# Performance work log

Hardware: AMD Instinct MI355X
Metric: run time of the kernel (lower is better)

Reference implementation:

```python
import jax, jax.numpy as jnp
import numpy as np

B, T = 64, 64
HUMAN, IN = 64, 8
HS, ES, K = 1024, 1024, 7
PSI_H, PSI_LR = 1024, 30

_PAR_SHAPES = [(HS, HS), (HS,), (IN, HS), (HS, HUMAN), (IN, HUMAN - IN)]
_PAR_SIZES = [int(np.prod(s)) for s in _PAR_SHAPES]
N_PSI = int(sum(_PAR_SIZES))
_OFFS = np.cumsum([0] + _PAR_SIZES)


def setup_inputs() -> dict:
    key = jax.random.key(0)
    ks = jax.random.split(key, 16)
    def xav(k, shape):
        lim = float(np.sqrt(6.0 / (shape[0] + shape[1])))
        return jax.random.uniform(k, shape, minval=-lim, maxval=lim, dtype=jnp.float32)
    def uni(k, shape, s):
        return jax.random.uniform(k, shape, minval=-s, maxval=s, dtype=jnp.float32)
    se = float(1.0 / np.sqrt(ES))
    return {
        "inputs": jax.random.normal(ks[0], (B, T, IN), jnp.float32),
        "outputs": jax.random.normal(ks[1], (B, T, HUMAN), jnp.float32),
        "eps": jax.random.normal(ks[2], (B, K), jnp.float32),
        "enc_Wih": uni(ks[3], (3 * ES, HUMAN), se),
        "enc_Whh": uni(ks[4], (3 * ES, ES), se),
        "enc_bih": uni(ks[5], (3 * ES,), se),
        "enc_bhh": uni(ks[6], (3 * ES,), se),
        "to_mu": xav(ks[7], (ES, K)),
        "to_lsigma": xav(ks[8], (ES, K)),
        "to_lsigma_bias": -0.5 * jnp.ones((K,), jnp.float32),
        "W1": xav(ks[9], (K, PSI_H)),
        "b1": jnp.zeros((PSI_H,), jnp.float32),
        "W2": xav(ks[10], (PSI_H, PSI_LR)),
        "b2": jnp.zeros((PSI_LR,), jnp.float32),
        "W3": xav(ks[11], (PSI_LR, N_PSI)),
        "b3": jnp.zeros((N_PSI,), jnp.float32),
        "gru_Wih": xav(ks[12], (IN, 2 * HS)),
        "gru_Whh": xav(ks[13], (HS, 2 * HS)),
        "gru_bias": jnp.concatenate([jnp.zeros((HS,)), jnp.ones((HS,))]).astype(jnp.float32),
    }


def _gru_cell(h, x, Wih, Whh, bih, bhh):
    # torch.nn.GRUCell math, gate order (r, z, n)
    gx = x @ Wih.T + bih
    gh = h @ Whh.T + bhh
    xr, xz, xn = jnp.split(gx, 3, axis=-1)
    hr, hz, hn = jnp.split(gh, 3, axis=-1)
    r = jax.nn.sigmoid(xr + hr)
    z = jax.nn.sigmoid(xz + hz)
    n = jnp.tanh(xn + r * hn)
    return (1.0 - z) * n + z * h


def _split_psi(psi):
    # psi: [B, N_PSI] -> per-sample (Whh, bh, Wih, C, D)
    return [psi[:, _OFFS[i]:_OFFS[i + 1]].reshape((-1,) + _PAR_SHAPES[i]) for i in range(5)]


def reference(inputs, outputs, eps, enc_Wih, enc_Whh, enc_bih, enc_bhh,
              to_mu, to_lsigma, to_lsigma_bias, W1, b1, W2, b2, W3, b3,
              gru_Wih, gru_Whh, gru_bias):
    bsz = inputs.shape[0]
    # ---- encoder: GRUCell over time-major outputs ----
    out_tm = jnp.swapaxes(outputs, 0, 1)  # [T, B, HUMAN]
    h0 = jnp.zeros((bsz, ES), inputs.dtype)
    h_enc = _gru_cell(h0, out_tm[0], enc_Wih, enc_Whh, enc_bih, enc_bhh)
    def enc_step(h, x):
        h = _gru_cell(h, x, enc_Wih, enc_Whh, enc_bih, enc_bhh)
        return h, None
    h_enc, _ = jax.lax.scan(enc_step, h_enc, out_tm[1:])
    mu = h_enc @ to_mu                       # [B, K]
    logstd = h_enc @ to_lsigma + to_lsigma_bias
    z = mu + eps * jnp.exp(logstd)
    # ---- hypernetwork psi decoder ----
    psi = (jnp.tanh(z @ W1 + b1) @ W2 + b2) @ W3 + b3   # [B, N_PSI]
    Whh_b, bh_b, Wih_b, C_b, D_b = _split_psi(psi)
    # ---- per-sample GRU decoder, vectorized over batch, scan over time ----
    gx_all = jnp.einsum('bti,ij->tbj', inputs, gru_Wih)  # [T, B, 2*HS]
    xW_all = jnp.einsum('bti,bih->tbh', inputs, Wih_b)   # [T, B, HS]

    def dec_step(h, xs):
        gx_t, xW_t = xs
        pre = gx_t + h @ gru_Whh + gru_bias   # [B, 2*HS]
        z_t = jax.nn.sigmoid(pre[:, :HS])
        r_t = jax.nn.sigmoid(pre[:, HS:])
        hWhh = jnp.einsum('bh,bhk->bk', h, Whh_b) + bh_b
        eta = jnp.tanh(xW_t + r_t * jnp.tanh(hWhh))
        h_new = z_t * h + (1.0 - z_t) * eta
        return h_new, h_new

    state0 = jnp.zeros((bsz, HS), inputs.dtype)
    h_last, dec_seq = jax.lax.scan(dec_step, state0, (gx_all, xW_all))
    dec_seq = jnp.swapaxes(dec_seq, 0, 1)    # [B, T, HS]
    # ---- readout ----
    yhats = jnp.einsum('bth,bhm->btm', dec_seq, C_b)
    xD = jnp.einsum('bti,bim->btm', inputs, D_b)  # [B, T, HUMAN-IN]
    yhats = yhats + jnp.concatenate([jnp.zeros_like(inputs), xD], axis=-1)
    # residual output
    yhats = yhats + jnp.concatenate(
        [inputs, jnp.zeros((bsz, inputs.shape[1], HUMAN - IN), inputs.dtype)], axis=-1)
    states = jax.lax.stop_gradient(h_last)
    return yhats, mu, logstd, states
```

## Files before the change

### kernel.cpp

```cpp
#include <hip/hip_runtime.h>

namespace {
constexpr int nT = 64;
constexpr int nK = 7;
constexpr long N_PSI = 1123776;
constexpr long SZ_WHH = 1048576;
constexpr long REST_SZ = 75200;
constexpr long R_BH = 0;
constexpr long R_WIH = 1024;
constexpr long R_C = 9216;
constexpr long R_D = 74752;
constexpr int NCH = 32;
constexpr int CHR = 32;
constexpr long PHALF = (long)NCH * 64 * 1024;
}

typedef __attribute__((ext_vector_type(4))) unsigned short us4;
typedef __attribute__((ext_vector_type(2))) unsigned short us2;

__device__ __forceinline__ float b2f(unsigned short u) {
  return __uint_as_float(((unsigned int)u) << 16);
}
__device__ __forceinline__ unsigned short f2b(float f) {
  unsigned int u = __float_as_uint(f);
  return (unsigned short)((u + 0x7fffu + ((u >> 16) & 1u)) >> 16);
}
__device__ __forceinline__ float sigm(float x) { return 1.f / (1.f + __expf(-x)); }

__global__ void transpose_bf16_k(const float* __restrict__ in, unsigned short* __restrict__ out,
                                 int rows, int cols) {
  __shared__ float tile[32][33];
  int x = blockIdx.x * 32 + threadIdx.x;
  int y = blockIdx.y * 32 + threadIdx.y;
  #pragma unroll
  for (int i = 0; i < 32; i += 8)
    if ((y + i) < rows && x < cols) tile[threadIdx.y + i][threadIdx.x] = in[(long)(y + i) * cols + x];
  __syncthreads();
  x = blockIdx.y * 32 + threadIdx.x;
  y = blockIdx.x * 32 + threadIdx.y;
  #pragma unroll
  for (int i = 0; i < 32; i += 8)
    if ((y + i) < cols && x < rows) out[(long)(y + i) * rows + x] = f2b(tile[threadIdx.x][threadIdx.y + i]);
}

__global__ void cvt_bf16_k(const float* __restrict__ in, unsigned short* __restrict__ out, long n) {
  long i = (long)blockIdx.x * 256 + threadIdx.x;
  if (i < n) out[i] = f2b(in[i]);
}

__global__ __launch_bounds__(256) void enc_gx_k(const float* __restrict__ outputs,
                                                const unsigned short* __restrict__ WtWihB,
                                                const float* __restrict__ bih,
                                                unsigned short* __restrict__ gxE) {
  int g0 = blockIdx.x * 256;
  int btg = blockIdx.y;
  __shared__ unsigned short ws[64 * 256];
  __shared__ float xs[64][64];
  for (int i = threadIdx.x; i < 64 * 256; i += 256)
    ws[i] = WtWihB[(long)(i >> 8) * 3072 + g0 + (i & 255)];
  for (int i = threadIdx.x; i < 64 * 64; i += 256) {
    int idx = btg * 64 + (i >> 6);
    int t = idx >> 6, b = idx & 63;
    xs[i >> 6][i & 63] = outputs[((long)b * nT + t) * 64 + (i & 63)];
  }
  __syncthreads();
  float bihv = bih[g0 + threadIdx.x];
  for (int j = 0; j < 64; ++j) {
    int idx = btg * 64 + j;
    float acc = bihv;
    #pragma unroll 8
    for (int i = 0; i < 64; ++i) acc += xs[j][i] * b2f(ws[i * 256 + threadIdx.x]);
    gxE[(long)idx * 3072 + g0 + threadIdx.x] = f2b(acc);
  }
}

__global__ __launch_bounds__(256) void dec_gx_k(const float* __restrict__ inputs,
                                                const float* __restrict__ gWih,
                                                const float* __restrict__ gbias,
                                                unsigned short* __restrict__ gxD) {
  int g0 = blockIdx.x * 256;
  int btg = blockIdx.y;
  __shared__ float ws[8][256];
  __shared__ float xs[64][8];
  for (int i = threadIdx.x; i < 8 * 256; i += 256)
    ws[i >> 8][i & 255] = gWih[(long)(i >> 8) * 2048 + g0 + (i & 255)];
  for (int i = threadIdx.x; i < 64 * 8; i += 256) {
    int idx = btg * 64 + (i >> 3);
    int t = idx >> 6, b = idx & 63;
    xs[i >> 3][i & 7] = inputs[((long)b * nT + t) * 8 + (i & 7)];
  }
  __syncthreads();
  float bv = gbias[g0 + threadIdx.x];
  for (int j = 0; j < 64; ++j) {
    int idx = btg * 64 + j;
    float acc = bv;
    #pragma unroll
    for (int i = 0; i < 8; ++i) acc += xs[j][i] * ws[i][threadIdx.x];
    gxD[(long)idx * 2048 + g0 + threadIdx.x] = f2b(acc);
  }
}

__global__ __launch_bounds__(256) void xW_k(const float* __restrict__ inputs,
                                            const float* __restrict__ Rest,
                                            unsigned short* __restrict__ xWb) {
  int k0 = blockIdx.x * 256;
  int b = blockIdx.y;
  __shared__ float ws[8][256];
  __shared__ float xs[64][8];
  const float* RB = Rest + (long)b * REST_SZ + R_WIH;
  for (int i = threadIdx.x; i < 8 * 256; i += 256)
    ws[i >> 8][i & 255] = RB[(long)(i >> 8) * 1024 + k0 + (i & 255)];
  for (int i = threadIdx.x; i < 64 * 8; i += 256)
    xs[i >> 3][i & 7] = inputs[((long)b * nT + (i >> 3)) * 8 + (i & 7)];
  __syncthreads();
  for (int t = 0; t < 64; ++t) {
    float acc = 0.f;
    #pragma unroll
    for (int i = 0; i < 8; ++i) acc += xs[t][i] * ws[i][threadIdx.x];
    xWb[((long)t * 64 + b) * 1024 + k0 + threadIdx.x] = f2b(acc);
  }
}

__global__ __launch_bounds__(256) void enc_step_k(
    const unsigned short* __restrict__ W,
    const unsigned short* __restrict__ gxE,
    const float* __restrict__ bhh,
    float* __restrict__ hEnc,
    const float* __restrict__ pRr, const float* __restrict__ pZr, const float* __restrict__ pNr,
    float* __restrict__ pRw, float* __restrict__ pZw, float* __restrict__ pNw,
    int t) {
  int c = blockIdx.x & (NCH - 1);
  int sp = blockIdx.x >> 5;
  int b0 = sp * 2, b1 = b0 + 1;
  __shared__ float h0s[CHR], h1s[CHR];
  __shared__ float redR[4][64], redZ[4][64], redN[4][64];

  int v = threadIdx.x;
  int q = v >> 6, idx = v & 63;
  {
    int hi = idx >> 5, e_in = idx & 31;
    int bb = hi ? b1 : b0;
    int e = c * CHR + e_in;
    float sr = 0.f, sz = 0.f, sn = 0.f;
    if (t > 0) {
      #pragma unroll
      for (int cc = q * 8; cc < q * 8 + 8; ++cc) {
        long base = ((long)cc * 64 + bb) * 1024 + e;
        sr += pRr[base]; sz += pZr[base]; sn += pNr[base];
      }
    }
    redR[q][idx] = sr; redZ[q][idx] = sz; redN[q][idx] = sn;
  }
  __syncthreads();
  if (v < 64) {
    int hi = v >> 5, e_in = v & 31;
    int bb = hi ? b1 : b0;
    int e = c * CHR + e_in;
    float sr = redR[0][v] + redR[1][v] + redR[2][v] + redR[3][v];
    float sz = redZ[0][v] + redZ[1][v] + redZ[2][v] + redZ[3][v];
    float sn = redN[0][v] + redN[1][v] + redN[2][v] + redN[3][v];
    long gb = ((long)t * 64 + bb) * 3072;
    float xr = b2f(gxE[gb + e]), xz = b2f(gxE[gb + 1024 + e]), xn = b2f(gxE[gb + 2048 + e]);
    float hr = sr + bhh[e], hz = sz + bhh[1024 + e], hn = sn + bhh[2048 + e];
    float r = sigm(xr + hr);
    float z = sigm(xz + hz);
    float n = tanhf(xn + r * hn);
    float hold = (t > 0) ? hEnc[(long)bb * 1024 + e] : 0.f;
    float hnew = (1.f - z) * n + z * hold;
    hEnc[(long)bb * 1024 + e] = hnew;
    if (hi) h1s[e_in] = hnew; else h0s[e_in] = hnew;
  }
  __syncthreads();

  if (t < nT - 1) {
    int e0 = threadIdx.x * 4;
    float ar0[4] = {}, az0[4] = {}, an0[4] = {}, ar1[4] = {}, az1[4] = {}, an1[4] = {};
    const unsigned short* Wb = W + (long)(c * CHR) * 3072 + e0;
    #pragma unroll 4
    for (int j = 0; j < CHR; ++j) {
      us4 wr = *(const us4*)(Wb + (long)j * 3072);
      us4 wz = *(const us4*)(Wb + (long)j * 3072 + 1024);
      us4 wn = *(const us4*)(Wb + (long)j * 3072 + 2048);
      float hv0 = h0s[j], hv1 = h1s[j];
      #pragma unroll
      for (int qq = 0; qq < 4; ++qq) {
        float fr = b2f(wr[qq]), fz = b2f(wz[qq]), fn = b2f(wn[qq]);
        ar0[qq] += hv0 * fr; az0[qq] += hv0 * fz; an0[qq] += hv0 * fn;
        ar1[qq] += hv1 * fr; az1[qq] += hv1 * fz; an1[qq] += hv1 * fn;
      }
    }
    long i0 = ((long)c * 64 + b0) * 1024 + e0;
    long i1 = i0 + 1024;
    *(float4*)(pRw + i0) = make_float4(ar0[0], ar0[1], ar0[2], ar0[3]);
    *(float4*)(pZw + i0) = make_float4(az0[0], az0[1], az0[2], az0[3]);
    *(float4*)(pNw + i0) = make_float4(an0[0], an0[1], an0[2], an0[3]);
    *(float4*)(pRw + i1) = make_float4(ar1[0], ar1[1], ar1[2], ar1[3]);
    *(float4*)(pZw + i1) = make_float4(az1[0], az1[1], az1[2], az1[3]);
    *(float4*)(pNw + i1) = make_float4(an1[0], an1[1], an1[2], an1[3]);
  }
}

__global__ __launch_bounds__(256) void latent_hyper_k(
    const float* __restrict__ h_enc,
    const float* __restrict__ to_mu, const float* __restrict__ to_lsig,
    const float* __restrict__ lsig_bias, const float* __restrict__ eps,
    const float* __restrict__ W1, const float* __restrict__ b1,
    const float* __restrict__ W2, const float* __restrict__ b2,
    float* __restrict__ out_mu, float* __restrict__ out_lsig,
    float* __restrict__ a2out) {
  int b = blockIdx.x;
  __shared__ float hs[1024];
  __shared__ float zv[8];
  __shared__ float a1[1024];
  for (int i = threadIdx.x; i < 1024; i += 256) hs[i] = h_enc[b * 1024 + i];
  __syncthreads();
  int g = threadIdx.x >> 5, s = threadIdx.x & 31;
  if (g < nK) {
    float am = 0.f, as_ = 0.f;
    for (int h = s; h < 1024; h += 32) {
      float hv = hs[h];
      am += hv * to_mu[h * nK + g];
      as_ += hv * to_lsig[h * nK + g];
    }
    #pragma unroll
    for (int m = 16; m >= 1; m >>= 1) { am += __shfl_xor(am, m); as_ += __shfl_xor(as_, m); }
    if (s == 0) {
      float ls = as_ + lsig_bias[g];
      out_mu[b * nK + g] = am;
      out_lsig[b * nK + g] = ls;
      zv[g] = am + eps[b * nK + g] * __expf(ls);
    }
  }
  __syncthreads();
  for (int j = threadIdx.x; j < 1024; j += 256) {
    float acc = b1[j];
    #pragma unroll
    for (int i = 0; i < nK; ++i) acc += zv[i] * W1[i * 1024 + j];
    a1[j] = tanhf(acc);
  }
  __syncthreads();
  int l = threadIdx.x >> 3, s8 = threadIdx.x & 7;
  if (l < 30) {
    float acc = 0.f;
    for (int j = s8; j < 1024; j += 8) acc += a1[j] * W2[j * 30 + l];
    acc += __shfl_xor(acc, 4);
    acc += __shfl_xor(acc, 2);
    acc += __shfl_xor(acc, 1);
    if (s8 == 0) a2out[b * 30 + l] = acc + b2[l];
  }
}

__global__ __launch_bounds__(256) void psi_k(const float* __restrict__ a2,
                                             const float* __restrict__ W3, const float* __restrict__ b3,
                                             unsigned short* __restrict__ WhhB, float* __restrict__ Rest) {
  __shared__ float sa[64 * 30];
  for (int i = threadIdx.x; i < 64 * 30; i += 256) sa[i] = a2[i];
  long n0 = ((long)blockIdx.x * 256 + threadIdx.x) * 2;
  __syncthreads();
  if (n0 >= N_PSI) return;
  float2 w[30];
  #pragma unroll
  for (int l = 0; l < 30; ++l) w[l] = *(const float2*)(W3 + (long)l * N_PSI + n0);
  float2 bb = *(const float2*)(b3 + n0);
  bool isWhh = (n0 < SZ_WHH);
  for (int b = 0; b < 64; ++b) {
    float a0 = bb.x, a1v = bb.y;
    const float* ab = &sa[b * 30];
    #pragma unroll
    for (int l = 0; l < 30; ++l) { float av = ab[l]; a0 += av * w[l].x; a1v += av * w[l].y; }
    if (isWhh) {
      us2 o; o[0] = f2b(a0); o[1] = f2b(a1v);
      *(us2*)(WhhB + (long)b * SZ_WHH + n0) = o;
    } else {
      *(float2*)(Rest + (long)b * REST_SZ + (n0 - SZ_WHH)) = make_float2(a0, a1v);
    }
  }
}

__global__ __launch_bounds__(256) void dec_step_k(
    const unsigned short* __restrict__ WhhB,
    const unsigned short* __restrict__ gWhhB,
    const unsigned short* __restrict__ gxD,
    const unsigned short* __restrict__ xWb,
    const float* __restrict__ Rest,
    float* __restrict__ decS,
    const float* __restrict__ pZr, const float* __restrict__ pRr, const float* __restrict__ pWr,
    float* __restrict__ pZw, float* __restrict__ pRw, float* __restrict__ pWw,
    int t) {
  int c = blockIdx.x & (NCH - 1);
  int sp = blockIdx.x >> 5;
  int b0 = sp * 2, b1 = b0 + 1;
  __shared__ float h0s[CHR], h1s[CHR];
  __shared__ float redZ[4][64], redR[4][64], redW[4][64];

  int v = threadIdx.x;
  int q = v >> 6, idx = v & 63;
  {
    int hi = idx >> 5, e_in = idx & 31;
    int bb = hi ? b1 : b0;
    int k = c * CHR + e_in;
    float sz = 0.f, sr = 0.f, sw = 0.f;
    if (t > 0) {
      #pragma unroll
      for (int cc = q * 8; cc < q * 8 + 8; ++cc) {
        long base = ((long)cc * 64 + bb) * 1024 + k;
        sz += pZr[base]; sr += pRr[base]; sw += pWr[base];
      }
    }
    redZ[q][idx] = sz; redR[q][idx] = sr; redW[q][idx] = sw;
  }
  __syncthreads();
  if (v < 64) {
    int hi = v >> 5, e_in = v & 31;
    int bb = hi ? b1 : b0;
    int k = c * CHR + e_in;
    float sz = redZ[0][v] + redZ[1][v] + redZ[2][v] + redZ[3][v];
    float sr = redR[0][v] + redR[1][v] + redR[2][v] + redR[3][v];
    float sw = redW[0][v] + redW[1][v] + redW[2][v] + redW[3][v];
    long gb = ((long)t * 64 + bb) * 2048;
    float gz = b2f(gxD[gb + k]), gr = b2f(gxD[gb + 1024 + k]);
    float z = sigm(gz + sz);
    float r = sigm(gr + sr);
    float hW = sw + Rest[(long)bb * REST_SZ + R_BH + k];
    float xw = b2f(xWb[((long)t * 64 + bb) * 1024 + k]);
    float eta = tanhf(xw + r * tanhf(hW));
    float hold = (t > 0) ? decS[((long)bb * nT + (t - 1)) * 1024 + k] : 0.f;
    float hnew = z * hold + (1.f - z) * eta;
    decS[((long)bb * nT + t) * 1024 + k] = hnew;
    if (hi) h1s[e_in] = hnew; else h0s[e_in] = hnew;
  }
  __syncthreads();

  if (t < nT - 1) {
    int k0 = threadIdx.x * 4;
    float az0[4] = {}, ar0[4] = {}, aw0[4] = {}, az1[4] = {}, ar1[4] = {}, aw1[4] = {};
    const unsigned short* G = gWhhB + (long)(c * CHR) * 2048 + k0;
    const unsigned short* W0 = WhhB + (long)b0 * SZ_WHH + (long)(c * CHR) * 1024 + k0;
    const unsigned short* W1p = WhhB + (long)b1 * SZ_WHH + (long)(c * CHR) * 1024 + k0;
    #pragma unroll 4
    for (int j = 0; j < CHR; ++j) {
      us4 wz = *(const us4*)(G + (long)j * 2048);
      us4 wr = *(const us4*)(G + (long)j * 2048 + 1024);
      us4 w0 = *(const us4*)(W0 + (long)j * 1024);
      us4 w1 = *(const us4*)(W1p + (long)j * 1024);
      float hv0 = h0s[j], hv1 = h1s[j];
      #pragma unroll
      for (int qq = 0; qq < 4; ++qq) {
        float fz = b2f(wz[qq]), fr = b2f(wr[qq]), f0 = b2f(w0[qq]), f1 = b2f(w1[qq]);
        az0[qq] += hv0 * fz; ar0[qq] += hv0 * fr; aw0[qq] += hv0 * f0;
        az1[qq] += hv1 * fz; ar1[qq] += hv1 * fr; aw1[qq] += hv1 * f1;
      }
    }
    long i0 = ((long)c * 64 + b0) * 1024 + k0;
    long i1 = i0 + 1024;
    *(float4*)(pZw + i0) = make_float4(az0[0], az0[1], az0[2], az0[3]);
    *(float4*)(pRw + i0) = make_float4(ar0[0], ar0[1], ar0[2], ar0[3]);
    *(float4*)(pWw + i0) = make_float4(aw0[0], aw0[1], aw0[2], aw0[3]);
    *(float4*)(pZw + i1) = make_float4(az1[0], az1[1], az1[2], az1[3]);
    *(float4*)(pRw + i1) = make_float4(ar1[0], ar1[1], ar1[2], ar1[3]);
    *(float4*)(pWw + i1) = make_float4(aw1[0], aw1[1], aw1[2], aw1[3]);
  }
}

__global__ __launch_bounds__(256) void readout_k(
    const float* __restrict__ dec_seq, const float* __restrict__ inputs,
    const float* __restrict__ Rest, float* __restrict__ yhats) {
  int b = blockIdx.x >> 3;
  int tg = blockIdx.x & 7;
  __shared__ float ss[8][1024];
  __shared__ float part[4][8][64];
  for (int i = threadIdx.x; i < 8 * 1024; i += 256)
    ss[i >> 10][i & 1023] = dec_seq[((long)b * nT + tg * 8 + (i >> 10)) * 1024 + (i & 1023)];
  __syncthreads();
  int m = threadIdx.x & 63, hq = threadIdx.x >> 6;
  const float* C = Rest + (long)b * REST_SZ + R_C;
  float acc[8] = {};
  for (int h = hq * 256; h < hq * 256 + 256; ++h) {
    float cv = C[(long)h * 64 + m];
    #pragma unroll
    for (int tt = 0; tt < 8; ++tt) acc[tt] += ss[tt][h] * cv;
  }
  #pragma unroll
  for (int tt = 0; tt < 8; ++tt) part[hq][tt][m] = acc[tt];
  __syncthreads();
  const float* D = Rest + (long)b * REST_SZ + R_D;
  for (int o = threadIdx.x; o < 512; o += 256) {
    int tt = o >> 6, mm = o & 63;
    float a = part[0][tt][mm] + part[1][tt][mm] + part[2][tt][mm] + part[3][tt][mm];
    long bt = (long)b * nT + tg * 8 + tt;
    if (mm < 8) {
      a += inputs[bt * 8 + mm];
    } else {
      #pragma unroll
      for (int i = 0; i < 8; ++i) a += inputs[bt * 8 + i] * D[i * 56 + (mm - 8)];
    }
    yhats[bt * 64 + mm] = a;
  }
}

__global__ void copy_states_k(const float* __restrict__ dec_seq, float* __restrict__ states) {
  int i = blockIdx.x * 256 + threadIdx.x;
  int b = i >> 10, h = i & 1023;
  states[i] = dec_seq[((long)b * nT + (nT - 1)) * 1024 + h];
}

extern "C" void kernel_launch(void* const* d_in, const int* in_sizes, int n_in,
                              void* d_out, int out_size, void* d_ws, size_t ws_size,
                              hipStream_t stream) {
  const float* inputs  = (const float*)d_in[0];
  const float* outputs = (const float*)d_in[1];
  const float* eps     = (const float*)d_in[2];
  const float* enc_Wih = (const float*)d_in[3];
  const float* enc_Whh = (const float*)d_in[4];
  const float* enc_bih = (const float*)d_in[5];
  const float* enc_bhh = (const float*)d_in[6];
  const float* to_mu   = (const float*)d_in[7];
  const float* to_lsig = (const float*)d_in[8];
  const float* lsig_b  = (const float*)d_in[9];
  const float* W1 = (const float*)d_in[10];
  const float* b1 = (const float*)d_in[11];
  const float* W2 = (const float*)d_in[12];
  const float* b2 = (const float*)d_in[13];
  const float* W3 = (const float*)d_in[14];
  const float* b3 = (const float*)d_in[15];
  const float* gWih  = (const float*)d_in[16];
  const float* gWhh  = (const float*)d_in[17];
  const float* gbias = (const float*)d_in[18];

  char* ws = (char*)d_ws;
  size_t off = 0;
  auto alloc = [&](size_t bytes) { size_t o = off; off = (off + bytes + 255) & ~(size_t)255; return o; };
  size_t oWhhB   = alloc(64ull * SZ_WHH * 2);
  size_t oRest   = alloc(64ull * REST_SZ * 4);
  size_t ogWhhB  = alloc(1024ull * 2048 * 2);
  size_t oWtWhhB = alloc(1024ull * 3072 * 2);
  size_t oWtWihB = alloc(64ull * 3072 * 2);
  size_t ogxE    = alloc(64ull * 64 * 3072 * 2);
  size_t ogxD    = alloc(64ull * 64 * 2048 * 2);
  size_t oxWb    = alloc(64ull * 64 * 1024 * 2);
  size_t opA     = alloc((size_t)2 * PHALF * 4);
  size_t opB     = alloc((size_t)2 * PHALF * 4);
  size_t opC     = alloc((size_t)2 * PHALF * 4);
  size_t ohA     = alloc(64ull * 1024 * 4);
  size_t oDec    = alloc(64ull * 64 * 1024 * 4);
  size_t oZ      = alloc(64 * nK * 4);
  size_t oA2     = alloc(64 * 30 * 4);
  (void)ws_size; (void)in_sizes; (void)n_in; (void)out_size; (void)oZ;

  unsigned short* WhhB   = (unsigned short*)(ws + oWhhB);
  float*          Rest   = (float*)(ws + oRest);
  unsigned short* gWhhB  = (unsigned short*)(ws + ogWhhB);
  unsigned short* WtWhhB = (unsigned short*)(ws + oWtWhhB);
  unsigned short* WtWihB = (unsigned short*)(ws + oWtWihB);
  unsigned short* gxE    = (unsigned short*)(ws + ogxE);
  unsigned short* gxD    = (unsigned short*)(ws + ogxD);
  unsigned short* xWb    = (unsigned short*)(ws + oxWb);
  float* pA   = (float*)(ws + opA);
  float* pB   = (float*)(ws + opB);
  float* pC   = (float*)(ws + opC);
  float* hA   = (float*)(ws + ohA);
  float* decS = (float*)(ws + oDec);
  float* a2   = (float*)(ws + oA2);

  float* out    = (float*)d_out;
  float* out_yh = out;
  float* out_mu = out + 262144;
  float* out_ls = out + 262144 + 448;
  float* out_st = out + 262144 + 896;

  transpose_bf16_k<<<dim3(32, 96), dim3(32, 8), 0, stream>>>(enc_Whh, WtWhhB, 3072, 1024);
  transpose_bf16_k<<<dim3(2, 96),  dim3(32, 8), 0, stream>>>(enc_Wih, WtWihB, 3072, 64);
  cvt_bf16_k<<<(int)((1024ull * 2048 + 255) / 256), 256, 0, stream>>>(gWhh, gWhhB, 1024 * 2048);

  enc_gx_k<<<dim3(12, 64), 256, 0, stream>>>(outputs, WtWihB, enc_bih, gxE);

  for (int t = 0; t < nT; ++t) {
    int rp = t & 1, wp = (t + 1) & 1;
    enc_step_k<<<1024, 256, 0, stream>>>(WtWhhB, gxE, enc_bhh, hA,
        pA + (size_t)rp * PHALF, pB + (size_t)rp * PHALF, pC + (size_t)rp * PHALF,
        pA + (size_t)wp * PHALF, pB + (size_t)wp * PHALF, pC + (size_t)wp * PHALF, t);
  }

  latent_hyper_k<<<64, 256, 0, stream>>>(hA, to_mu, to_lsig, lsig_b, eps,
                                         W1, b1, W2, b2, out_mu, out_ls, a2);
  psi_k<<<(int)((N_PSI / 2 + 255) / 256), 256, 0, stream>>>(a2, W3, b3, WhhB, Rest);

  dec_gx_k<<<dim3(8, 64), 256, 0, stream>>>(inputs, gWih, gbias, gxD);
  xW_k<<<dim3(4, 64), 256, 0, stream>>>(inputs, Rest, xWb);

  for (int t = 0; t < nT; ++t) {
    int rp = t & 1, wp = (t + 1) & 1;
    dec_step_k<<<1024, 256, 0, stream>>>(WhhB, gWhhB, gxD, xWb, Rest, decS,
        pA + (size_t)rp * PHALF, pB + (size_t)rp * PHALF, pC + (size_t)rp * PHALF,
        pA + (size_t)wp * PHALF, pB + (size_t)wp * PHALF, pC + (size_t)wp * PHALF, t);
  }

  readout_k<<<512, 256, 0, stream>>>(decS, inputs, Rest, out_yh);
  copy_states_k<<<256, 256, 0, stream>>>(decS, out_st);
}
```

Measured before the change: 3.401 ms.

## Quantize per-sample decoder Whh to int8 and retile recurrent step kernels

The generated per-sample recurrent weight matrix Whh goes from bf16 to int8, with one scale per (sample, input row). The scales come from a separate max-abs pass over the hypernetwork output, and the scale is folded into h before the matvec. This halves the bytes streamed for the dominant per-step weight read in the decoder. Both encoder and decoder step kernels also move from 32 chunks of 32 rows at 256 threads to 16 chunks of 64 rows at 512 threads, with gate work split across two thread halves, which halves the partial-sum traffic. The cost is an extra psi pass that recomputes the hypernetwork matmul, plus quantization error in the decoder weights.

```diff
diff --git a/kernel.cpp b/kernel.cpp
--- a/kernel.cpp
+++ b/kernel.cpp
@@ -10,13 +10,11 @@
 constexpr long R_WIH = 1024;
 constexpr long R_C = 9216;
 constexpr long R_D = 74752;
-constexpr int NCH = 32;
-constexpr int CHR = 32;
+constexpr int NCH = 16;
 constexpr long PHALF = (long)NCH * 64 * 1024;
 }
 
 typedef __attribute__((ext_vector_type(4))) unsigned short us4;
-typedef __attribute__((ext_vector_type(2))) unsigned short us2;
 
 __device__ __forceinline__ float b2f(unsigned short u) {
   return __uint_as_float(((unsigned int)u) << 16);
@@ -121,7 +119,7 @@
   }
 }
 
-__global__ __launch_bounds__(256) void enc_step_k(
+__global__ __launch_bounds__(512, 2) void enc_step3_k(
     const unsigned short* __restrict__ W,
     const unsigned short* __restrict__ gxE,
     const float* __restrict__ bhh,
@@ -130,35 +128,33 @@
     float* __restrict__ pRw, float* __restrict__ pZw, float* __restrict__ pNw,
     int t) {
   int c = blockIdx.x & (NCH - 1);
-  int sp = blockIdx.x >> 5;
+  int sp = blockIdx.x >> 4;
   int b0 = sp * 2, b1 = b0 + 1;
-  __shared__ float h0s[CHR], h1s[CHR];
-  __shared__ float redR[4][64], redZ[4][64], redN[4][64];
-
+  __shared__ float h0s[64], h1s[64];
+  __shared__ float red[3][4][128];
   int v = threadIdx.x;
-  int q = v >> 6, idx = v & 63;
   {
-    int hi = idx >> 5, e_in = idx & 31;
-    int bb = hi ? b1 : b0;
-    int e = c * CHR + e_in;
+    int q = v >> 7, idx = v & 127;
+    int bb = (idx >> 6) ? b1 : b0;
+    int e = c * 64 + (idx & 63);
     float sr = 0.f, sz = 0.f, sn = 0.f;
     if (t > 0) {
       #pragma unroll
-      for (int cc = q * 8; cc < q * 8 + 8; ++cc) {
+      for (int cc = q * 4; cc < q * 4 + 4; ++cc) {
         long base = ((long)cc * 64 + bb) * 1024 + e;
         sr += pRr[base]; sz += pZr[base]; sn += pNr[base];
       }
     }
-    redR[q][idx] = sr; redZ[q][idx] = sz; redN[q][idx] = sn;
-  }
-  __syncthreads();
-  if (v < 64) {
-    int hi = v >> 5, e_in = v & 31;
+    red[0][q][idx] = sr; red[1][q][idx] = sz; red[2][q][idx] = sn;
+  }
+  __syncthreads();
+  if (v < 128) {
+    int hi = v >> 6;
     int bb = hi ? b1 : b0;
-    int e = c * CHR + e_in;
-    float sr = redR[0][v] + redR[1][v] + redR[2][v] + redR[3][v];
-    float sz = redZ[0][v] + redZ[1][v] + redZ[2][v] + redZ[3][v];
-    float sn = redN[0][v] + redN[1][v] + redN[2][v] + redN[3][v];
+    int e = c * 64 + (v & 63);
+    float sr = red[0][0][v] + red[0][1][v] + red[0][2][v] + red[0][3][v];
+    float sz = red[1][0][v] + red[1][1][v] + red[1][2][v] + red[1][3][v];
+    float sn = red[2][0][v] + red[2][1][v] + red[2][2][v] + red[2][3][v];
     long gb = ((long)t * 64 + bb) * 3072;
     float xr = b2f(gxE[gb + e]), xz = b2f(gxE[gb + 1024 + e]), xn = b2f(gxE[gb + 2048 + e]);
     float hr = sr + bhh[e], hz = sz + bhh[1024 + e], hn = sn + bhh[2048 + e];
@@ -168,35 +164,51 @@
     float hold = (t > 0) ? hEnc[(long)bb * 1024 + e] : 0.f;
     float hnew = (1.f - z) * n + z * hold;
     hEnc[(long)bb * 1024 + e] = hnew;
-    if (hi) h1s[e_in] = hnew; else h0s[e_in] = hnew;
-  }
-  __syncthreads();
-
+    if (hi) h1s[v & 63] = hnew; else h0s[v & 63] = hnew;
+  }
+  __syncthreads();
   if (t < nT - 1) {
-    int e0 = threadIdx.x * 4;
-    float ar0[4] = {}, az0[4] = {}, an0[4] = {}, ar1[4] = {}, az1[4] = {}, an1[4] = {};
-    const unsigned short* Wb = W + (long)(c * CHR) * 3072 + e0;
-    #pragma unroll 4
-    for (int j = 0; j < CHR; ++j) {
-      us4 wr = *(const us4*)(Wb + (long)j * 3072);
-      us4 wz = *(const us4*)(Wb + (long)j * 3072 + 1024);
-      us4 wn = *(const us4*)(Wb + (long)j * 3072 + 2048);
-      float hv0 = h0s[j], hv1 = h1s[j];
-      #pragma unroll
-      for (int qq = 0; qq < 4; ++qq) {
-        float fr = b2f(wr[qq]), fz = b2f(wz[qq]), fn = b2f(wn[qq]);
-        ar0[qq] += hv0 * fr; az0[qq] += hv0 * fz; an0[qq] += hv0 * fn;
-        ar1[qq] += hv1 * fr; az1[qq] += hv1 * fz; an1[qq] += hv1 * fn;
+    if (v < 256) {
+      int e0 = v * 4;
+      float ar0[4] = {}, az0[4] = {}, ar1[4] = {}, az1[4] = {};
+      const unsigned short* Wb = W + (long)(c * 64) * 3072 + e0;
+      #pragma unroll 4
+      for (int j = 0; j < 64; ++j) {
+        us4 wr = *(const us4*)(Wb + (long)j * 3072);
+        us4 wz = *(const us4*)(Wb + (long)j * 3072 + 1024);
+        float hv0 = h0s[j], hv1 = h1s[j];
+        #pragma unroll
+        for (int q = 0; q < 4; ++q) {
+          float fr = b2f(wr[q]), fz = b2f(wz[q]);
+          ar0[q] += hv0 * fr; az0[q] += hv0 * fz;
+          ar1[q] += hv1 * fr; az1[q] += hv1 * fz;
+        }
       }
-    }
-    long i0 = ((long)c * 64 + b0) * 1024 + e0;
-    long i1 = i0 + 1024;
-    *(float4*)(pRw + i0) = make_float4(ar0[0], ar0[1], ar0[2], ar0[3]);
-    *(float4*)(pZw + i0) = make_float4(az0[0], az0[1], az0[2], az0[3]);
-    *(float4*)(pNw + i0) = make_float4(an0[0], an0[1], an0[2], an0[3]);
-    *(float4*)(pRw + i1) = make_float4(ar1[0], ar1[1], ar1[2], ar1[3]);
-    *(float4*)(pZw + i1) = make_float4(az1[0], az1[1], az1[2], az1[3]);
-    *(float4*)(pNw + i1) = make_float4(an1[0], an1[1], an1[2], an1[3]);
+      long i0 = ((long)c * 64 + b0) * 1024 + e0;
+      long i1 = i0 + 1024;
+      *(float4*)(pRw + i0) = make_float4(ar0[0], ar0[1], ar0[2], ar0[3]);
+      *(float4*)(pZw + i0) = make_float4(az0[0], az0[1], az0[2], az0[3]);
+      *(float4*)(pRw + i1) = make_float4(ar1[0], ar1[1], ar1[2], ar1[3]);
+      *(float4*)(pZw + i1) = make_float4(az1[0], az1[1], az1[2], az1[3]);
+    } else {
+      int e0 = (v - 256) * 4;
+      float an0[4] = {}, an1[4] = {};
+      const unsigned short* Wb = W + (long)(c * 64) * 3072 + 2048 + e0;
+      #pragma unroll 8
+      for (int j = 0; j < 64; ++j) {
+        us4 wn = *(const us4*)(Wb + (long)j * 3072);
+        float hv0 = h0s[j], hv1 = h1s[j];
+        #pragma unroll
+        for (int q = 0; q < 4; ++q) {
+          float fn = b2f(wn[q]);
+          an0[q] += hv0 * fn; an1[q] += hv1 * fn;
+        }
+      }
+      long i0 = ((long)c * 64 + b0) * 1024 + e0;
+      long i1 = i0 + 1024;
+      *(float4*)(pNw + i0) = make_float4(an0[0], an0[1], an0[2], an0[3]);
+      *(float4*)(pNw + i1) = make_float4(an1[0], an1[1], an1[2], an1[3]);
+    }
   }
 }
 
@@ -250,35 +262,84 @@
   }
 }
 
-__global__ __launch_bounds__(256) void psi_k(const float* __restrict__ a2,
-                                             const float* __restrict__ W3, const float* __restrict__ b3,
-                                             unsigned short* __restrict__ WhhB, float* __restrict__ Rest) {
+__global__ __launch_bounds__(256) void psi_max_k(
+    const float* __restrict__ a2, const float* __restrict__ W3, const float* __restrict__ b3,
+    unsigned* __restrict__ pmax) {
+  __shared__ float sa[64 * 30];
+  __shared__ float wm[4][64];
+  for (int i = threadIdx.x; i < 64 * 30; i += 256) sa[i] = a2[i];
+  long n0 = (long)blockIdx.x * 256 + threadIdx.x;
+  int h = (int)(n0 >> 10);
+  __syncthreads();
+  float acc[64];
+  float bb = b3[n0];
+  #pragma unroll
+  for (int b = 0; b < 64; ++b) acc[b] = bb;
+  for (int l = 0; l < 30; ++l) {
+    float w = W3[(long)l * N_PSI + n0];
+    #pragma unroll
+    for (int b = 0; b < 64; ++b) acc[b] += sa[b * 30 + l] * w;
+  }
+  int lane = threadIdx.x & 63, wv = threadIdx.x >> 6;
+  #pragma unroll
+  for (int b = 0; b < 64; ++b) {
+    float m = fabsf(acc[b]);
+    #pragma unroll
+    for (int d = 32; d >= 1; d >>= 1) m = fmaxf(m, __shfl_xor(m, d));
+    if (lane == 0) wm[wv][b] = m;
+  }
+  __syncthreads();
+  if (threadIdx.x < 64) {
+    int b = threadIdx.x;
+    float m = fmaxf(fmaxf(wm[0][b], wm[1][b]), fmaxf(wm[2][b], wm[3][b]));
+    atomicMax(&pmax[b * 1024 + h], __float_as_uint(m));
+  }
+}
+
+__global__ void wscale2_k(const unsigned* __restrict__ pmax,
+                          float* __restrict__ sdec, float* __restrict__ sinv) {
+  int i = blockIdx.x * 256 + threadIdx.x;
+  float m = __uint_as_float(pmax[i]);
+  sdec[i] = m / 127.f;
+  sinv[i] = (m > 0.f) ? 127.f / m : 0.f;
+}
+
+__global__ __launch_bounds__(256) void psi_q_k(
+    const float* __restrict__ a2, const float* __restrict__ W3, const float* __restrict__ b3,
+    const float* __restrict__ sinv, char* __restrict__ Q8, float* __restrict__ Rest) {
   __shared__ float sa[64 * 30];
   for (int i = threadIdx.x; i < 64 * 30; i += 256) sa[i] = a2[i];
-  long n0 = ((long)blockIdx.x * 256 + threadIdx.x) * 2;
+  long n0 = (long)blockIdx.x * 256 + threadIdx.x;
   __syncthreads();
   if (n0 >= N_PSI) return;
-  float2 w[30];
+  float acc[64];
+  float bb = b3[n0];
   #pragma unroll
-  for (int l = 0; l < 30; ++l) w[l] = *(const float2*)(W3 + (long)l * N_PSI + n0);
-  float2 bb = *(const float2*)(b3 + n0);
-  bool isWhh = (n0 < SZ_WHH);
-  for (int b = 0; b < 64; ++b) {
-    float a0 = bb.x, a1v = bb.y;
-    const float* ab = &sa[b * 30];
-    #pragma unroll
-    for (int l = 0; l < 30; ++l) { float av = ab[l]; a0 += av * w[l].x; a1v += av * w[l].y; }
-    if (isWhh) {
-      us2 o; o[0] = f2b(a0); o[1] = f2b(a1v);
-      *(us2*)(WhhB + (long)b * SZ_WHH + n0) = o;
-    } else {
-      *(float2*)(Rest + (long)b * REST_SZ + (n0 - SZ_WHH)) = make_float2(a0, a1v);
-    }
-  }
-}
-
-__global__ __launch_bounds__(256) void dec_step_k(
-    const unsigned short* __restrict__ WhhB,
+  for (int b = 0; b < 64; ++b) acc[b] = bb;
+  for (int l = 0; l < 30; ++l) {
+    float w = W3[(long)l * N_PSI + n0];
+    #pragma unroll
+    for (int b = 0; b < 64; ++b) acc[b] += sa[b * 30 + l] * w;
+  }
+  if (n0 < SZ_WHH) {
+    int h = (int)(n0 >> 10);
+    const float* si = sinv + h;
+    #pragma unroll
+    for (int b = 0; b < 64; ++b) {
+      int q = __float2int_rn(acc[b] * si[b * 1024]);
+      q = min(127, max(-127, q));
+      Q8[(long)b * SZ_WHH + n0] = (char)q;
+    }
+  } else {
+    long r = n0 - SZ_WHH;
+    #pragma unroll
+    for (int b = 0; b < 64; ++b) Rest[(long)b * REST_SZ + r] = acc[b];
+  }
+}
+
+__global__ __launch_bounds__(512, 2) void dec_step_q8d_k(
+    const char* __restrict__ Q8,
+    const float* __restrict__ sdec,
     const unsigned short* __restrict__ gWhhB,
     const unsigned short* __restrict__ gxD,
     const unsigned short* __restrict__ xWb,
@@ -288,35 +349,34 @@
     float* __restrict__ pZw, float* __restrict__ pRw, float* __restrict__ pWw,
     int t) {
   int c = blockIdx.x & (NCH - 1);
-  int sp = blockIdx.x >> 5;
+  int sp = blockIdx.x >> 4;
   int b0 = sp * 2, b1 = b0 + 1;
-  __shared__ float h0s[CHR], h1s[CHR];
-  __shared__ float redZ[4][64], redR[4][64], redW[4][64];
-
+  __shared__ float h0s[64], h1s[64];
+  __shared__ float h0q[64], h1q[64];
+  __shared__ float red[3][4][128];
   int v = threadIdx.x;
-  int q = v >> 6, idx = v & 63;
   {
-    int hi = idx >> 5, e_in = idx & 31;
-    int bb = hi ? b1 : b0;
-    int k = c * CHR + e_in;
+    int q = v >> 7, idx = v & 127;
+    int bb = (idx >> 6) ? b1 : b0;
+    int k = c * 64 + (idx & 63);
     float sz = 0.f, sr = 0.f, sw = 0.f;
     if (t > 0) {
       #pragma unroll
-      for (int cc = q * 8; cc < q * 8 + 8; ++cc) {
+      for (int cc = q * 4; cc < q * 4 + 4; ++cc) {
         long base = ((long)cc * 64 + bb) * 1024 + k;
         sz += pZr[base]; sr += pRr[base]; sw += pWr[base];
       }
     }
-    redZ[q][idx] = sz; redR[q][idx] = sr; redW[q][idx] = sw;
-  }
-  __syncthreads();
-  if (v < 64) {
-    int hi = v >> 5, e_in = v & 31;
+    red[0][q][idx] = sz; red[1][q][idx] = sr; red[2][q][idx] = sw;
+  }
+  __syncthreads();
+  if (v < 128) {
+    int hi = v >> 6;
     int bb = hi ? b1 : b0;
-    int k = c * CHR + e_in;
-    float sz = redZ[0][v] + redZ[1][v] + redZ[2][v] + redZ[3][v];
-    float sr = redR[0][v] + redR[1][v] + redR[2][v] + redR[3][v];
-    float sw = redW[0][v] + redW[1][v] + redW[2][v] + redW[3][v];
+    int k = c * 64 + (v & 63);
+    float sz = red[0][0][v] + red[0][1][v] + red[0][2][v] + red[0][3][v];
+    float sr = red[1][0][v] + red[1][1][v] + red[1][2][v] + red[1][3][v];
+    float sw = red[2][0][v] + red[2][1][v] + red[2][2][v] + red[2][3][v];
     long gb = ((long)t * 64 + bb) * 2048;
     float gz = b2f(gxD[gb + k]), gr = b2f(gxD[gb + 1024 + k]);
     float z = sigm(gz + sz);
@@ -327,38 +387,54 @@
     float hold = (t > 0) ? decS[((long)bb * nT + (t - 1)) * 1024 + k] : 0.f;
     float hnew = z * hold + (1.f - z) * eta;
     decS[((long)bb * nT + t) * 1024 + k] = hnew;
-    if (hi) h1s[e_in] = hnew; else h0s[e_in] = hnew;
-  }
-  __syncthreads();
-
+    float hsc = hnew * sdec[(long)bb * 1024 + k];
+    if (hi) { h1s[v & 63] = hnew; h1q[v & 63] = hsc; }
+    else    { h0s[v & 63] = hnew; h0q[v & 63] = hsc; }
+  }
+  __syncthreads();
   if (t < nT - 1) {
-    int k0 = threadIdx.x * 4;
-    float az0[4] = {}, ar0[4] = {}, aw0[4] = {}, az1[4] = {}, ar1[4] = {}, aw1[4] = {};
-    const unsigned short* G = gWhhB + (long)(c * CHR) * 2048 + k0;
-    const unsigned short* W0 = WhhB + (long)b0 * SZ_WHH + (long)(c * CHR) * 1024 + k0;
-    const unsigned short* W1p = WhhB + (long)b1 * SZ_WHH + (long)(c * CHR) * 1024 + k0;
-    #pragma unroll 4
-    for (int j = 0; j < CHR; ++j) {
-      us4 wz = *(const us4*)(G + (long)j * 2048);
-      us4 wr = *(const us4*)(G + (long)j * 2048 + 1024);
-      us4 w0 = *(const us4*)(W0 + (long)j * 1024);
-      us4 w1 = *(const us4*)(W1p + (long)j * 1024);
-      float hv0 = h0s[j], hv1 = h1s[j];
-      #pragma unroll
-      for (int qq = 0; qq < 4; ++qq) {
-        float fz = b2f(wz[qq]), fr = b2f(wr[qq]), f0 = b2f(w0[qq]), f1 = b2f(w1[qq]);
-        az0[qq] += hv0 * fz; ar0[qq] += hv0 * fr; aw0[qq] += hv0 * f0;
-        az1[qq] += hv1 * fz; ar1[qq] += hv1 * fr; aw1[qq] += hv1 * f1;
+    if (v < 256) {
+      int k0 = v * 4;
+      float az0[4] = {}, ar0[4] = {}, az1[4] = {}, ar1[4] = {};
+      const unsigned short* G = gWhhB + (long)(c * 64) * 2048 + k0;
+      #pragma unroll 4
+      for (int j = 0; j < 64; ++j) {
+        us4 wz = *(const us4*)(G + (long)j * 2048);
+        us4 wr = *(const us4*)(G + (long)j * 2048 + 1024);
+        float hv0 = h0s[j], hv1 = h1s[j];
+        #pragma unroll
+        for (int q = 0; q < 4; ++q) {
+          float fz = b2f(wz[q]), fr = b2f(wr[q]);
+          az0[q] += hv0 * fz; ar0[q] += hv0 * fr;
+          az1[q] += hv1 * fz; ar1[q] += hv1 * fr;
+        }
       }
-    }
-    long i0 = ((long)c * 64 + b0) * 1024 + k0;
-    long i1 = i0 + 1024;
-    *(float4*)(pZw + i0) = make_float4(az0[0], az0[1], az0[2], az0[3]);
-    *(float4*)(pRw + i0) = make_float4(ar0[0], ar0[1], ar0[2], ar0[3]);
-    *(float4*)(pWw + i0) = make_float4(aw0[0], aw0[1], aw0[2], aw0[3]);
-    *(float4*)(pZw + i1) = make_float4(az1[0], az1[1], az1[2], az1[3]);
-    *(float4*)(pRw + i1) = make_float4(ar1[0], ar1[1], ar1[2], ar1[3]);
-    *(float4*)(pWw + i1) = make_float4(aw1[0], aw1[1], aw1[2], aw1[3]);
+      long i0 = ((long)c * 64 + b0) * 1024 + k0;
+      long i1 = i0 + 1024;
+      *(float4*)(pZw + i0) = make_float4(az0[0], az0[1], az0[2], az0[3]);
+      *(float4*)(pRw + i0) = make_float4(ar0[0], ar0[1], ar0[2], ar0[3]);
+      *(float4*)(pZw + i1) = make_float4(az1[0], az1[1], az1[2], az1[3]);
+      *(float4*)(pRw + i1) = make_float4(ar1[0], ar1[1], ar1[2], ar1[3]);
+    } else {
+      int k0 = (v - 256) * 4;
+      float aw0[4] = {}, aw1[4] = {};
+      const char* Q0 = Q8 + (long)b0 * SZ_WHH + (long)(c * 64) * 1024 + k0;
+      const char* Q1 = Q8 + (long)b1 * SZ_WHH + (long)(c * 64) * 1024 + k0;
+      #pragma unroll 8
+      for (int j = 0; j < 64; ++j) {
+        char4 q0 = *(const char4*)(Q0 + (long)j * 1024);
+        char4 q1 = *(const char4*)(Q1 + (long)j * 1024);
+        float hv0 = h0q[j], hv1 = h1q[j];
+        aw0[0] += hv0 * (float)q0.x; aw0[1] += hv0 * (float)q0.y;
+        aw0[2] += hv0 * (float)q0.z; aw0[3] += hv0 * (float)q0.w;
+        aw1[0] += hv1 * (float)q1.x; aw1[1] += hv1 * (float)q1.y;
+        aw1[2] += hv1 * (float)q1.z; aw1[3] += hv1 * (float)q1.w;
+      }
+      long i0 = ((long)c * 64 + b0) * 1024 + k0;
+      long i1 = i0 + 1024;
+      *(float4*)(pWw + i0) = make_float4(aw0[0], aw0[1], aw0[2], aw0[3]);
+      *(float4*)(pWw + i1) = make_float4(aw1[0], aw1[1], aw1[2], aw1[3]);
+    }
   }
 }
 
@@ -430,8 +506,8 @@
   char* ws = (char*)d_ws;
   size_t off = 0;
   auto alloc = [&](size_t bytes) { size_t o = off; off = (off + bytes + 255) & ~(size_t)255; return o; };
-  size_t oWhhB   = alloc(64ull * SZ_WHH * 2);
   size_t oRest   = alloc(64ull * REST_SZ * 4);
+  size_t oQ8     = alloc(64ull * SZ_WHH);
   size_t ogWhhB  = alloc(1024ull * 2048 * 2);
   size_t oWtWhhB = alloc(1024ull * 3072 * 2);
   size_t oWtWihB = alloc(64ull * 3072 * 2);
@@ -443,12 +519,14 @@
   size_t opC     = alloc((size_t)2 * PHALF * 4);
   size_t ohA     = alloc(64ull * 1024 * 4);
   size_t oDec    = alloc(64ull * 64 * 1024 * 4);
-  size_t oZ      = alloc(64 * nK * 4);
   size_t oA2     = alloc(64 * 30 * 4);
-  (void)ws_size; (void)in_sizes; (void)n_in; (void)out_size; (void)oZ;
-
-  unsigned short* WhhB   = (unsigned short*)(ws + oWhhB);
+  size_t oPmax   = alloc(64ull * 1024 * 4);
+  size_t oSdec   = alloc(64ull * 1024 * 4);
+  size_t oSinv   = alloc(64ull * 1024 * 4);
+  (void)in_sizes; (void)n_in; (void)out_size; (void)ws_size;
+
   float*          Rest   = (float*)(ws + oRest);
+  char*           Q8     = (char*)(ws + oQ8);
   unsigned short* gWhhB  = (unsigned short*)(ws + ogWhhB);
   unsigned short* WtWhhB = (unsigned short*)(ws + oWtWhhB);
   unsigned short* WtWihB = (unsigned short*)(ws + oWtWihB);
@@ -461,6 +539,9 @@
   float* hA   = (float*)(ws + ohA);
   float* decS = (float*)(ws + oDec);
   float* a2   = (float*)(ws + oA2);
+  unsigned* pmax = (unsigned*)(ws + oPmax);
+  float* sdec = (float*)(ws + oSdec);
+  float* sinv = (float*)(ws + oSinv);
 
   float* out    = (float*)d_out;
   float* out_yh = out;
@@ -468,6 +549,8 @@
   float* out_ls = out + 262144 + 448;
   float* out_st = out + 262144 + 896;
 
+  hipMemsetAsync(pmax, 0, 64ull * 1024 * 4, stream);
+
   transpose_bf16_k<<<dim3(32, 96), dim3(32, 8), 0, stream>>>(enc_Whh, WtWhhB, 3072, 1024);
   transpose_bf16_k<<<dim3(2, 96),  dim3(32, 8), 0, stream>>>(enc_Wih, WtWihB, 3072, 64);
   cvt_bf16_k<<<(int)((1024ull * 2048 + 255) / 256), 256, 0, stream>>>(gWhh, gWhhB, 1024 * 2048);
@@ -476,21 +559,23 @@
 
   for (int t = 0; t < nT; ++t) {
     int rp = t & 1, wp = (t + 1) & 1;
-    enc_step_k<<<1024, 256, 0, stream>>>(WtWhhB, gxE, enc_bhh, hA,
+    enc_step3_k<<<512, 512, 0, stream>>>(WtWhhB, gxE, enc_bhh, hA,
         pA + (size_t)rp * PHALF, pB + (size_t)rp * PHALF, pC + (size_t)rp * PHALF,
         pA + (size_t)wp * PHALF, pB + (size_t)wp * PHALF, pC + (size_t)wp * PHALF, t);
   }
 
   latent_hyper_k<<<64, 256, 0, stream>>>(hA, to_mu, to_lsig, lsig_b, eps,
                                          W1, b1, W2, b2, out_mu, out_ls, a2);
-  psi_k<<<(int)((N_PSI / 2 + 255) / 256), 256, 0, stream>>>(a2, W3, b3, WhhB, Rest);
+  psi_max_k<<<(int)(SZ_WHH / 256), 256, 0, stream>>>(a2, W3, b3, pmax);
+  wscale2_k<<<256, 256, 0, stream>>>(pmax, sdec, sinv);
+  psi_q_k<<<(int)((N_PSI + 255) / 256), 256, 0, stream>>>(a2, W3, b3, sinv, Q8, Rest);
 
   dec_gx_k<<<dim3(8, 64), 256, 0, stream>>>(inputs, gWih, gbias, gxD);
   xW_k<<<dim3(4, 64), 256, 0, stream>>>(inputs, Rest, xWb);
 
   for (int t = 0; t < nT; ++t) {
     int rp = t & 1, wp = (t + 1) & 1;
-    dec_step_k<<<1024, 256, 0, stream>>>(WhhB, gWhhB, gxD, xWb, Rest, decS,
+    dec_step_q8d_k<<<512, 512, 0, stream>>>(Q8, sdec, gWhhB, gxD, xWb, Rest, decS,
         pA + (size_t)rp * PHALF, pB + (size_t)rp * PHALF, pC + (size_t)rp * PHALF,
         pA + (size_t)wp * PHALF, pB + (size_t)wp * PHALF, pC + (size_t)wp * PHALF, t);
   }
```

Result: faster. 2.995 ms (-11.9%).
